# Kernel tuning notes

Measured on AMD Instinct MI355X. Metric: run time of the kernel, lower is better.

The kernel has to match this reference:

```python
import jax, jax.numpy as jnp
import numpy as np

B, C_IN, C_OUT, H, W, OH, OW, K = 2, 8, 16, 512, 1024, 512, 1024, 9


def setup_inputs() -> dict:
    key = jax.random.key(0)
    k1, k2, k3, k4 = jax.random.split(key, 4)
    x = jax.random.normal(k1, (B, C_IN, H, W), dtype=jnp.float32)
    # sample_map holds (x, y) float pixel coords; scale rand [0,1) into bounds
    sm = jax.random.uniform(k2, (OH, OW, K, 2), dtype=jnp.float32)
    sample_map = sm * jnp.array([W - 1.0, H - 1.0], dtype=jnp.float32)
    n = C_IN * K
    stdv = 1.0 / np.sqrt(n)
    weight = jax.random.uniform(k3, (C_OUT, C_IN, K), dtype=jnp.float32,
                                minval=-stdv, maxval=stdv)
    bias = jax.random.uniform(k4, (C_OUT,), dtype=jnp.float32,
                              minval=-stdv, maxval=stdv)
    return {"x": x, "sample_map": sample_map, "weight": weight, "bias": bias}


def _bilinear_sample(x, sample_map):
    # x: [B,C,H,W]; sample_map: [OH,OW,K,2] with (px, py)
    b, c, h, w = x.shape
    px = sample_map[..., 0]  # [OH,OW,K]
    py = sample_map[..., 1]
    x0 = jnp.floor(px)
    y0 = jnp.floor(py)
    wx = px - x0
    wy = py - y0
    x0i = jnp.clip(x0.astype(jnp.int32), 0, w - 1)
    x1i = jnp.clip(x0i + 1, 0, w - 1)
    y0i = jnp.clip(y0.astype(jnp.int32), 0, h - 1)
    y1i = jnp.clip(y0i + 1, 0, h - 1)
    x_flat = x.reshape(b, c, h * w)

    def gather(yi, xi):
        flat = (yi * w + xi).reshape(-1)
        g = jnp.take(x_flat, flat, axis=2)
        return g.reshape(b, c, *yi.shape)  # [B,C,OH,OW,K]

    wx = wx[None, None]
    wy = wy[None, None]
    sampled = ((1 - wy) * (1 - wx) * gather(y0i, x0i)
               + (1 - wy) * wx * gather(y0i, x1i)
               + wy * (1 - wx) * gather(y1i, x0i)
               + wy * wx * gather(y1i, x1i))
    return sampled  # [B,C,OH,OW,K]


def reference(x, sample_map, weight, bias):
    sampled = _bilinear_sample(x, sample_map)          # [B,C,OH,OW,K]
    out = jnp.einsum('bchwk,ock->bohw', sampled, weight)
    return out + bias[None, :, None, None]
```

## Files before the change

kernel.cpp:

```cpp
#include <hip/hip_runtime.h>

#define BB   2
#define CIN  8
#define COUT 16
#define HH   512
#define WW   1024
#define KK   9
#define NPIX (HH*WW)
#define COPY4 (1u << 20)

typedef unsigned int u32;
typedef float f32x4 __attribute__((ext_vector_type(4)));
typedef float f32x2 __attribute__((ext_vector_type(2)));

#define SB() __builtin_amdgcn_sched_barrier(0)

__device__ __forceinline__ u32 f2bf(float f) {
  u32 u = __float_as_uint(f);
  return (u + 0x7fffu + ((u >> 16) & 1u)) >> 16;
}
__device__ __forceinline__ float bflo(u32 u) { return __uint_as_float(u << 16); }
__device__ __forceinline__ float bfhi(u32 u) { return __uint_as_float(u & 0xffff0000u); }
__device__ __forceinline__ u32 comp4(uint4 v, int j) {
  return j == 0 ? v.x : j == 1 ? v.y : j == 2 ? v.z : v.w;
}


__global__ __launch_bounds__(256) void xpose3c_k(const float* __restrict__ x,
                                                 uint4* __restrict__ xt4) {
  int t = blockIdx.x * 256 + threadIdx.x;
  if (t >= (HH / 2) * (WW / 2) * BB) return;
  int b  = t & 1;
  int s  = t >> 1;
  int by = s >> 9;
  int bx = s & 511;

  u32 pk[3][3][4];
  #pragma unroll
  for (int j = 0; j < 4; ++j) {
    const float* c0 = x + (size_t)(b * CIN + 2 * j    ) * NPIX;
    const float* c1 = x + (size_t)(b * CIN + 2 * j + 1) * NPIX;
    int i1 = min(bx + 1, WW / 2 - 1);
    #pragma unroll
    for (int r = 0; r < 3; ++r) {
      int row = min(2 * by + r, HH - 1);
      const float2* p0 = (const float2*)(c0 + (size_t)row * WW);
      const float2* p1 = (const float2*)(c1 + (size_t)row * WW);
      float2 a0 = p0[bx], a1 = p0[i1];
      float2 b0 = p1[bx], b1 = p1[i1];
      pk[r][0][j] = f2bf(a0.x) | (f2bf(b0.x) << 16);
      pk[r][1][j] = f2bf(a0.y) | (f2bf(b0.y) << 16);
      pk[r][2][j] = f2bf(a1.x) | (f2bf(b1.x) << 16);
    }
  }

  #pragma unroll
  for (int pyp = 0; pyp < 2; ++pyp)
    #pragma unroll
    for (int pxp = 0; pxp < 2; ++pxp) {
      u32 base = ((u32)(pyp * 2 + pxp) << 20)
               + ((u32)(by * 512 + bx) * 2 + (u32)b) * 4;
      #pragma unroll
      for (int d = 0; d < 4; ++d) {
        int dy = d >> 1, dx = d & 1;
        uint4 v;
        v.x = pk[pyp + dy][pxp + dx][0];
        v.y = pk[pyp + dy][pxp + dx][1];
        v.z = pk[pyp + dy][pxp + dx][2];
        v.w = pk[pyp + dy][pxp + dx][3];
        xt4[base + d] = v;
      }
    }
}

__global__ __launch_bounds__(256) void mconv9_k(const uint4* __restrict__ xt4,
                                                const float* __restrict__ sm,
                                                const float* __restrict__ weight,
                                                const float* __restrict__ bias,
                                                float* __restrict__ out) {
  __shared__ float sml[128 * KK * 2];
  __shared__ float wlds[KK * CIN * COUT];

  int tid = threadIdx.x;
  {
    const f32x4* g = (const f32x4*)(sm + (size_t)blockIdx.x * 128 * KK * 2);
    f32x4* l = (f32x4*)sml;
    for (int i = tid; i < 128 * KK * 2 / 4; i += 256) l[i] = g[i];
  }
  for (int i = tid; i < KK * CIN * COUT; i += 256) {
    int k = i >> 7, c = (i >> 4) & 7, o = i & 15;
    wlds[i] = weight[(o * CIN + c) * KK + k];
  }
  __syncthreads();

  const int b  = tid & 1;
  const int pl = tid >> 1;
  const int p  = blockIdx.x * 128 + pl;

  f32x2 acc2[8];
  #pragma unroll
  for (int o2 = 0; o2 < 8; ++o2) { acc2[o2][0] = bias[2*o2]; acc2[o2][1] = bias[2*o2+1]; }

  const float2* smp = (const float2*)sml + pl * KK;

  auto LOADK = [&](int k, uint4 (&v)[4]) {
    float2 s = smp[k];
    int x0 = min(max((int)floorf(s.x), 0), WW - 2);
    int y0 = min(max((int)floorf(s.y), 0), HH - 2);
    u32 idx = ((u32)((y0 & 1) * 2 + (x0 & 1)) << 20)
            + ((u32)((y0 >> 1) * 512 + (x0 >> 1)) * 2 + (u32)b) * 4;
    v[0] = xt4[idx];     v[1] = xt4[idx + 1];
    v[2] = xt4[idx + 2]; v[3] = xt4[idx + 3];
  };

  auto CONS = [&](int k, uint4 (&v)[4]) {
    float2 s = smp[k];
    float x0f = floorf(s.x), y0f = floorf(s.y);
    float wx = s.x - x0f, wy = s.y - y0f;
    float w00 = (1.f - wy) * (1.f - wx), w01 = (1.f - wy) * wx;
    float w10 = wy * (1.f - wx),         w11 = wy * wx;
    const float4* w4 = (const float4*)&wlds[k * (CIN * COUT)];

    float sv[8];
    #pragma unroll
    for (int j = 0; j < 4; ++j) {
      u32 a00 = comp4(v[0], j), a01 = comp4(v[1], j);
      u32 a10 = comp4(v[2], j), a11 = comp4(v[3], j);
      sv[2*j]   = w00*bflo(a00) + w01*bflo(a01) + w10*bflo(a10) + w11*bflo(a11);
      sv[2*j+1] = w00*bfhi(a00) + w01*bfhi(a01) + w10*bfhi(a10) + w11*bfhi(a11);
    }
    #pragma unroll
    for (int c = 0; c < 8; ++c) {
      float s0 = sv[c];
      #pragma unroll
      for (int og = 0; og < 4; ++og) {
        float4 wv = w4[c * 4 + og];
        f32x2 wlo; wlo[0] = wv.x; wlo[1] = wv.y;
        f32x2 whi; whi[0] = wv.z; whi[1] = wv.w;
        acc2[og*2]   += wlo * s0;
        acc2[og*2+1] += whi * s0;
      }
    }
  };

  uint4 va[4], vb[4], vc[4], vd[4];
  LOADK(0, va); LOADK(1, vb); LOADK(2, vc); LOADK(3, vd); SB();
  CONS(0, va);  SB(); LOADK(4, va); SB();
  CONS(1, vb);  SB(); LOADK(5, vb); SB();
  CONS(2, vc);  SB(); LOADK(6, vc); SB();
  CONS(3, vd);  SB(); LOADK(7, vd); SB();
  CONS(4, va);  SB(); LOADK(8, va); SB();
  CONS(5, vb);  SB();
  CONS(6, vc);  SB();
  CONS(7, vd);  SB();
  CONS(8, va);

  #pragma unroll
  for (int o2 = 0; o2 < 8; ++o2) {
    __builtin_nontemporal_store(acc2[o2][0], &out[(size_t)(b * COUT + 2*o2    ) * NPIX + p]);
    __builtin_nontemporal_store(acc2[o2][1], &out[(size_t)(b * COUT + 2*o2 + 1) * NPIX + p]);
  }
}

__global__ __launch_bounds__(256) void mconv_direct_k(const float* __restrict__ x,
                                                      const float* __restrict__ sm,
                                                      const float* __restrict__ weight,
                                                      const float* __restrict__ bias,
                                                      float* __restrict__ out) {
  __shared__ float wlds[KK * CIN * COUT];
  int tid = threadIdx.x;
  for (int i = tid; i < KK * CIN * COUT; i += 256) {
    int k = i >> 7, c = (i >> 4) & 7, o = i & 15;
    wlds[i] = weight[(o * CIN + c) * KK + k];
  }
  __syncthreads();

  int p = blockIdx.x * 256 + tid;
  if (p >= NPIX) return;

  float acc[2][COUT];
  #pragma unroll
  for (int o = 0; o < COUT; ++o) { float bv = bias[o]; acc[0][o] = bv; acc[1][o] = bv; }

  const float2* smp = (const float2*)sm;

  for (int k = 0; k < KK; ++k) {
    float2 s = smp[(size_t)p * KK + k];
    float x0f = floorf(s.x), y0f = floorf(s.y);
    float wx = s.x - x0f, wy = s.y - y0f;
    int x0 = min(max((int)x0f, 0), WW - 1);
    int y0 = min(max((int)y0f, 0), HH - 1);
    int x1 = min(x0 + 1, WW - 1), y1 = min(y0 + 1, HH - 1);
    float w00 = (1.f - wy) * (1.f - wx), w01 = (1.f - wy) * wx;
    float w10 = wy * (1.f - wx),         w11 = wy * wx;

    float sv[2][8];
    #pragma unroll
    for (int b = 0; b < 2; ++b) {
      #pragma unroll
      for (int c = 0; c < 8; ++c) {
        const float* xp = x + (size_t)(b * CIN + c) * NPIX;
        float v00 = xp[y0 * WW + x0], v01 = xp[y0 * WW + x1];
        float v10 = xp[y1 * WW + x0], v11 = xp[y1 * WW + x1];
        sv[b][c] = w00 * v00 + w01 * v01 + w10 * v10 + w11 * v11;
      }
    }

    const float4* w4 = (const float4*)&wlds[k * (CIN * COUT)];
    #pragma unroll
    for (int c = 0; c < 8; ++c) {
      float s0 = sv[0][c], s1 = sv[1][c];
      #pragma unroll
      for (int og = 0; og < 4; ++og) {
        float4 wv = w4[c * 4 + og];
        acc[0][og*4+0] += s0 * wv.x; acc[1][og*4+0] += s1 * wv.x;
        acc[0][og*4+1] += s0 * wv.y; acc[1][og*4+1] += s1 * wv.y;
        acc[0][og*4+2] += s0 * wv.z; acc[1][og*4+2] += s1 * wv.z;
        acc[0][og*4+3] += s0 * wv.w; acc[1][og*4+3] += s1 * wv.w;
      }
    }
  }

  #pragma unroll
  for (int b = 0; b < 2; ++b)
    #pragma unroll
    for (int o = 0; o < COUT; ++o)
      out[(size_t)(b * COUT + o) * NPIX + p] = acc[b][o];
}

extern "C" void kernel_launch(void* const* d_in, const int* in_sizes, int n_in,
                              void* d_out, int out_size, void* d_ws, size_t ws_size,
                              hipStream_t stream) {
  const float* x      = (const float*)d_in[0];
  const float* sm     = (const float*)d_in[1];
  const float* weight = (const float*)d_in[2];
  const float* bias   = (const float*)d_in[3];
  float* out = (float*)d_out;

  const size_t oneCopy = (size_t)COPY4 * sizeof(uint4);
  uint4* xt4 = (uint4*)d_ws;
  if (ws_size >= 4 * oneCopy) {
    hipLaunchKernelGGL(xpose3c_k, dim3((HH / 2) * (WW / 2) * BB / 256), dim3(256), 0,
                       stream, x, xt4);
    hipLaunchKernelGGL(mconv9_k, dim3(NPIX / 128), dim3(256), 0, stream,
                       xt4, sm, weight, bias, out);
  } else {
    hipLaunchKernelGGL(mconv_direct_k, dim3((NPIX + 255) / 256), dim3(256), 0, stream,
                       x, sm, weight, bias, out);
  }
}
```

Measured before the change: 139.1 us.

## Rewrite bf16 quad-layout transpose kernel with LDS-tiled 32x32 staging

Replaces the per-thread transpose, which read float2 pairs straight from global memory, with a block-tiled kernel. Each block loads a 33x33 pixel halo tile for both batches into shared memory as packed bf16 channel vectors. It then writes the four parity copies of 2x2 neighbourhoods with coalesced uint4 stores. The aim is to cut redundant and uncoalesced global reads in the preprocessing pass, at the cost of a 33x66 uint4 LDS tile (about 35 KB) that limits occupancy, plus one halo row and column per tile.

```diff
diff --git a/kernel.cpp b/kernel.cpp
--- a/kernel.cpp
+++ b/kernel.cpp
@@ -26,51 +26,52 @@
 }
 
 
-__global__ __launch_bounds__(256) void xpose3c_k(const float* __restrict__ x,
-                                                 uint4* __restrict__ xt4) {
-  int t = blockIdx.x * 256 + threadIdx.x;
-  if (t >= (HH / 2) * (WW / 2) * BB) return;
-  int b  = t & 1;
-  int s  = t >> 1;
-  int by = s >> 9;
-  int bx = s & 511;
-
-  u32 pk[3][3][4];
-  #pragma unroll
-  for (int j = 0; j < 4; ++j) {
-    const float* c0 = x + (size_t)(b * CIN + 2 * j    ) * NPIX;
-    const float* c1 = x + (size_t)(b * CIN + 2 * j + 1) * NPIX;
-    int i1 = min(bx + 1, WW / 2 - 1);
-    #pragma unroll
-    for (int r = 0; r < 3; ++r) {
-      int row = min(2 * by + r, HH - 1);
-      const float2* p0 = (const float2*)(c0 + (size_t)row * WW);
-      const float2* p1 = (const float2*)(c1 + (size_t)row * WW);
-      float2 a0 = p0[bx], a1 = p0[i1];
-      float2 b0 = p1[bx], b1 = p1[i1];
-      pk[r][0][j] = f2bf(a0.x) | (f2bf(b0.x) << 16);
-      pk[r][1][j] = f2bf(a0.y) | (f2bf(b0.y) << 16);
-      pk[r][2][j] = f2bf(a1.x) | (f2bf(b1.x) << 16);
-    }
-  }
-
-  #pragma unroll
-  for (int pyp = 0; pyp < 2; ++pyp)
-    #pragma unroll
-    for (int pxp = 0; pxp < 2; ++pxp) {
-      u32 base = ((u32)(pyp * 2 + pxp) << 20)
-               + ((u32)(by * 512 + bx) * 2 + (u32)b) * 4;
-      #pragma unroll
-      for (int d = 0; d < 4; ++d) {
-        int dy = d >> 1, dx = d & 1;
-        uint4 v;
-        v.x = pk[pyp + dy][pxp + dx][0];
-        v.y = pk[pyp + dy][pxp + dx][1];
-        v.z = pk[pyp + dy][pxp + dx][2];
-        v.w = pk[pyp + dy][pxp + dx][3];
-        xt4[base + d] = v;
-      }
-    }
+__global__ __launch_bounds__(256) void xpose4_k(const float* __restrict__ x,
+                                                uint4* __restrict__ xt4) {
+  __shared__ uint4 lds_px[33 * 2 * 33];
+
+  const int tile = blockIdx.x;
+  const int ty = tile >> 5;
+  const int tx = tile & 31;
+  const int tid = threadIdx.x;
+
+  for (int e = tid; e < 33 * 33 * 2; e += 256) {
+    int py  = e / 66;
+    int rem = e - py * 66;
+    int b   = rem >= 33;
+    int px  = rem - (b ? 33 : 0);
+    int gy = min(ty * 32 + py, HH - 1);
+    int gx = min(tx * 32 + px, WW - 1);
+    const float* base = x + (size_t)gy * WW + gx;
+    u32 pk[4];
+    #pragma unroll
+    for (int j = 0; j < 4; ++j) {
+      float f0 = base[(size_t)(b * CIN + 2 * j    ) * NPIX];
+      float f1 = base[(size_t)(b * CIN + 2 * j + 1) * NPIX];
+      pk[j] = f2bf(f0) | (f2bf(f1) << 16);
+    }
+    uint4 v; v.x = pk[0]; v.y = pk[1]; v.z = pk[2]; v.w = pk[3];
+    lds_px[e] = v;
+  }
+  __syncthreads();
+
+  #pragma unroll
+  for (int it = 0; it < 32; ++it) {
+    int w   = it * 256 + tid;
+    int d   = w & 3;
+    int b   = (w >> 2) & 1;
+    int bxl = (w >> 3) & 15;
+    int oyp = (w >> 7) & 15;
+    int c   = (w >> 11) & 3;
+    int pyp = c >> 1, pxp = c & 1;
+    int row = 2 * oyp + pyp + (d >> 1);
+    int col = 2 * bxl + pxp + (d & 1);
+    uint4 v = lds_px[(row * 2 + b) * 33 + col];
+    u32 by_g = (u32)(ty * 16 + oyp);
+    u32 bx_g = (u32)(tx * 16 + bxl);
+    u32 addr = ((u32)c << 20) + ((by_g * 512 + bx_g) * 2 + (u32)b) * 4 + (u32)d;
+    xt4[addr] = v;
+  }
 }
 
 __global__ __launch_bounds__(256) void mconv9_k(const uint4* __restrict__ xt4,
@@ -240,7 +241,7 @@
   const size_t oneCopy = (size_t)COPY4 * sizeof(uint4);
   uint4* xt4 = (uint4*)d_ws;
   if (ws_size >= 4 * oneCopy) {
-    hipLaunchKernelGGL(xpose3c_k, dim3((HH / 2) * (WW / 2) * BB / 256), dim3(256), 0,
+    hipLaunchKernelGGL(xpose4_k, dim3((HH / 32) * (WW / 32)), dim3(256), 0,
                        stream, x, xt4);
     hipLaunchKernelGGL(mconv9_k, dim3(NPIX / 128), dim3(256), 0, stream,
                        xt4, sm, weight, bias, out);
```

Result: faster. 126.2 us (-9.2%).
